# Performance work log

Hardware: AMD Instinct MI355X
Metric: run time of the kernel (lower is better)

The kernel has to match this reference:

```python
import jax, jax.numpy as jnp
import numpy as np
from jax import lax

S, U, T, F = 64, 10, 160, 80       # speakers, utterances, frames, mel features
H, P, E, L = 768, 256, 256, 3      # hidden, proj, embedding, layers


def setup_inputs() -> dict:
    key = jax.random.key(0)
    ks = iter(jax.random.split(key, 32))
    s = 0.05
    d = {"x": jax.random.normal(next(ks), (S, U, T, F), jnp.float32)}
    for l in range(L):
        fin = F if l == 0 else P
        d[f"W_ih{l}"] = jax.random.normal(next(ks), (4 * H, fin), jnp.float32) * s
        d[f"W_hh{l}"] = jax.random.normal(next(ks), (4 * H, P), jnp.float32) * s
        d[f"b_ih{l}"] = jax.random.normal(next(ks), (4 * H,), jnp.float32) * s
        d[f"b_hh{l}"] = jax.random.normal(next(ks), (4 * H,), jnp.float32) * s
        d[f"W_hr{l}"] = jax.random.normal(next(ks), (P, H), jnp.float32) * s
    d["W_lin"] = jax.random.normal(next(ks), (E, P), jnp.float32) * s
    d["b_lin"] = jax.random.normal(next(ks), (E,), jnp.float32) * s
    return d


def _lstm_layer(x, Wih, Whh, bih, bhh, Whr):
    """Projected LSTM layer (PyTorch proj_size semantics, gate order i,f,g,o).
    x: [B, T, Fin] -> (outputs [B, T, P], final h [B, P])."""
    B = x.shape[0]
    # precompute input contribution for all timesteps: [T, B, 4H]
    pre = jnp.einsum('btf,gf->tbg', x, Wih) + bih + bhh

    def step(carry, pre_t):
        h, c = carry
        g = pre_t + h @ Whh.T                     # [B, 4H]
        i, f, gg, o = jnp.split(g, 4, axis=-1)
        c = jax.nn.sigmoid(f) * c + jax.nn.sigmoid(i) * jnp.tanh(gg)
        h = (jax.nn.sigmoid(o) * jnp.tanh(c)) @ Whr.T  # project H -> P
        return (h, c), h

    init = (jnp.zeros((B, P), x.dtype), jnp.zeros((B, H), x.dtype))
    (h_last, _), hs = lax.scan(step, init, pre)
    return jnp.transpose(hs, (1, 0, 2)), h_last


def reference(x, W_ih0, W_hh0, b_ih0, b_hh0, W_hr0,
              W_ih1, W_hh1, b_ih1, b_hh1, W_hr1,
              W_ih2, W_hh2, b_ih2, b_hh2, W_hr2,
              W_lin, b_lin):
    layers = [(W_ih0, W_hh0, b_ih0, b_hh0, W_hr0),
              (W_ih1, W_hh1, b_ih1, b_hh1, W_hr1),
              (W_ih2, W_hh2, b_ih2, b_hh2, W_hr2)]
    seq = x.reshape(-1, x.shape[2], x.shape[3])  # [S*U, T, F]
    h_last = None
    for (Wih, Whh, bih, bhh, Whr) in layers:
        seq, h_last = _lstm_layer(seq, Wih, Whh, bih, bhh, Whr)
    out = jax.nn.relu(h_last @ W_lin.T + b_lin)  # [S*U, E]
    norm = jnp.linalg.norm(out, axis=1, keepdims=True)
    out = out / jnp.maximum(norm, 1e-12)         # F.normalize(p=2, dim=1)
    return out.reshape(x.shape[0], x.shape[1], -1)  # [S, U, E]
```

## Files before the change

kernel.cpp:

```cpp
#include <hip/hip_runtime.h>
#include <stdint.h>

#define Sn 64
#define Un 10
#define Tn 160
#define Fn 80
#define Bn 640
#define Hn 768
#define Pn 256
#define En 256
#define G4H 3072
#define NBLK 480

using short8  = __attribute__((ext_vector_type(8))) short;
using short4v = __attribute__((ext_vector_type(4))) short;
using floatx4 = __attribute__((ext_vector_type(4))) float;

__device__ __forceinline__ short f2bf(float f){
    unsigned u = __builtin_bit_cast(unsigned, f);
    u += 0x7fffu + ((u >> 16) & 1u);
    return (short)(u >> 16);
}
__device__ __forceinline__ float bf2f(short s){
    return __builtin_bit_cast(float, ((unsigned)(unsigned short)s) << 16);
}
__device__ __forceinline__ float sigm(float x){ return 1.f / (1.f + __expf(-x)); }
__device__ __forceinline__ float tanh_(float x){
    float e = __expf(-2.f * fmaxf(x, -40.f));
    return (1.f - e) / (1.f + e);
}

__device__ __forceinline__ void gll(const short* g, short* l){
    __builtin_amdgcn_global_load_lds(
        (const __attribute__((address_space(1))) unsigned int*)(const void*)g,
        (__attribute__((address_space(3))) unsigned int*)(void*)l, 16, 0, 0);
}
#define VMW(N) asm volatile("s_waitcnt vmcnt(" #N ")" ::: "memory")
#define LGKM0  asm volatile("s_waitcnt lgkmcnt(0)" ::: "memory")


__global__ void k_prep(const float* __restrict__ Wih0,
                       const float* bi0, const float* bh0,
                       const float* bi1, const float* bh1,
                       const float* bi2, const float* bh2,
                       short* __restrict__ B0, float* __restrict__ bias){
    int i = blockIdx.x * 256 + threadIdx.x;
    const int W0 = G4H * 96;
    if (i < W0){
        int g = i / 96, c = i % 96;
        int gg = g / 768, jj = g % 768;
        int ct = jj / 48, r = jj % 48, ntB = r / 16, lnB = r % 16;
        int k = 768 + c, s = k >> 5, lq = (k >> 3) & 3, e = k & 7;
        size_t off = ((((size_t)(ct * 27 + s)) * 4 + gg) * 3 + ntB) * 512
                   + (size_t)(lq * 16 + lnB) * 8 + e;
        B0[off] = (c < Fn) ? f2bf(Wih0[(size_t)g * Fn + c]) : (short)0;
    } else if (i < W0 + 3 * G4H){
        int j = i - W0; int l = j / G4H, g = j % G4H;
        const float* a = (l == 0) ? bi0 : (l == 1) ? bi1 : bi2;
        const float* b = (l == 0) ? bh0 : (l == 1) ? bh1 : bh2;
        bias[j] = a[g] + b[g];
    }
}

__global__ void k_init(short* __restrict__ hidden, float* __restrict__ c){
    int i = blockIdx.x * 256 + threadIdx.x;
    int stride = gridDim.x * 256;
    const int NH = 3 * 2 * Bn * Hn;
    const int NC = 3 * Bn * Hn;
    for (int j = i; j < NH; j += stride) hidden[j] = 0;
    for (int j = i; j < NC; j += stride) c[j] = 0.f;
}

__global__ void k_fold(const float* __restrict__ A, const float* __restrict__ Whr,
                       short* __restrict__ out, int ldout, int coloff, int Mtiles,
                       int nstg){
    int mt = blockIdx.x % Mtiles, nt = blockIdx.x / Mtiles;
    int lane = threadIdx.x & 63;
    int ln = lane & 15, lq = lane >> 4;
    floatx4 acc = {0.f, 0.f, 0.f, 0.f};
    const float* ap = A + (size_t)(mt * 16 + ln) * 256 + lq * 8;
    const float* bp = Whr + (size_t)(lq * 8) * 768 + nt * 16 + ln;
    for (int p0 = 0; p0 < 256; p0 += 32){
        short8 af, bf;
        #pragma unroll
        for (int j = 0; j < 8; ++j) af[j] = f2bf(ap[p0 + j]);
        #pragma unroll
        for (int j = 0; j < 8; ++j) bf[j] = f2bf(bp[(size_t)(p0 + j) * 768]);
        acc = __builtin_amdgcn_mfma_f32_16x16x32_bf16(af, bf, acc, 0, 0, 0);
    }
    #pragma unroll
    for (int r = 0; r < 4; ++r){
        int row = mt * 16 + lq * 4 + r, col = nt * 16 + ln;
        int k = coloff + col;
        if (nstg){
            int gg = row / 768, jj = row % 768;
            int ct = jj / 48, rr = jj % 48, ntB = rr / 16, lnB = rr % 16;
            int s = k >> 5, lqk = (k >> 3) & 3, e = k & 7;
            size_t off = ((((size_t)ct * nstg + s) * 4 + gg) * 3 + ntB) * 512
                       + (size_t)(lqk * 16 + lnB) * 8 + e;
            out[off] = f2bf(acc[r]);
        } else {
            out[(size_t)row * ldout + k] = f2bf(acc[r]);
        }
    }
}

__global__ __launch_bounds__(256, 2) void k_step(const float* __restrict__ x,
        const short* __restrict__ B0, const short* __restrict__ B1,
        const short* __restrict__ B2, const float* __restrict__ bias,
        short* __restrict__ hidden, float* __restrict__ c, int w){
    __shared__ __align__(16) char smem[25088];
    short* sAr = (short*)smem;
    float* sEx = (float*)smem;

    const int tid = threadIdx.x, lane = tid & 63, wg = tid >> 6;
    const int bid = blockIdx.x;
    const int layer = bid % 3;
    const int t = w - layer;
    if (t < 0 || t >= Tn) return;
    const int r2 = bid / 3;
    const int mt = r2 >> 4, ct = r2 & 15;
    const int m0 = mt * 64, j0 = ct * 48;
    const short* Bl = (layer == 0) ? B0 : (layer == 1) ? B1 : B2;
    const int NSTG = (layer == 0) ? 27 : 48;
    const int ln = lane & 15, lq = lane >> 4;
    const int rr = tid >> 2;
    const int pp = (w + 1) & 1;

    const short* bglane = Bl + (size_t)lane * 8;
    const int ctb = ct * NSTG;

    int aoffA[3];
    #pragma unroll
    for (int j = 0; j < 3; ++j){
        int u = (wg * 3 + j) * 64 + lane;
        int row = u / 12, kcp = u % 12;
        int kcg = kcp - (row % 12); if (kcg < 0) kcg += 12;
        aoffA[j] = row * 96 + kcg * 8;
    }
    int prem[4];
    #pragma unroll
    for (int m4 = 0; m4 < 4; ++m4) prem[m4] = (m4 * 16 + ln) % 12;

    const short* srcA = (layer == 0) ? hidden + (size_t)pp * Bn * Hn
                       : hidden + (size_t)((layer - 1) * 2 + pp) * Bn * Hn;
    const short* srcH = hidden + (size_t)(layer * 2 + pp) * Bn * Hn;

    short8 bfr[3][3];

#define LOADB(s_, slot_)                                                        \
    {                                                                           \
        const short* p_ = bglane + (size_t)(((ctb) + (s_)) * 12 + wg * 3) * 512;\
        asm volatile("global_load_dwordx4 %0, %1, off"                          \
                     : "=v"(bfr[slot_][0]) : "v"(p_) : "memory");               \
        asm volatile("global_load_dwordx4 %0, %1, off offset:1024"              \
                     : "=v"(bfr[slot_][1]) : "v"(p_) : "memory");               \
        asm volatile("global_load_dwordx4 %0, %1, off offset:2048"              \
                     : "=v"(bfr[slot_][2]) : "v"(p_) : "memory");               \
    }

    auto issueA = [&](int chn){
        const short* src; int chg;
        if (layer == 0 || chn < 8){ src = srcA; chg = chn; }
        else { src = srcH; chg = chn - 8; }
        const short* gb = src + (size_t)(mt * 8 + chg) * 6144;
        #pragma unroll
        for (int j = 0; j < 3; ++j)
            gll(gb + aoffA[j], &sAr[(chn & 1) * 6144 + (wg * 3 + j) * 512]);
    };

    floatx4 acc[4][3];
    #pragma unroll
    for (int nt = 0; nt < 3; ++nt){
        float bv = bias[layer * G4H + wg * Hn + j0 + nt * 16 + ln];
        #pragma unroll
        for (int m4 = 0; m4 < 4; ++m4){
            acc[m4][nt][0] = bv; acc[m4][nt][1] = bv;
            acc[m4][nt][2] = bv; acc[m4][nt][3] = bv;
        }
    }

#define PH(k_, WAITN, ISSUE)                                                    \
    {                                                                           \
        VMW(WAITN);                                                             \
        __builtin_amdgcn_sched_barrier(0);                                      \
        short8 afr[4];                                                          \
        const int ksl_ = (k_) * 4 + lq;                                         \
        _Pragma("unroll")                                                       \
        for (int m4 = 0; m4 < 4; ++m4){                                         \
            int idx = prem[m4] + ksl_; if (idx >= 12) idx -= 12;                \
            afr[m4] = *(const short8*)&sAr[abuf * 6144 + ((m4 * 16 + ln) * 12 + idx) * 8]; \
        }                                                                       \
        _Pragma("unroll")                                                       \
        for (int m4 = 0; m4 < 4; ++m4)                                          \
            _Pragma("unroll")                                                   \
            for (int nt = 0; nt < 3; ++nt)                                      \
                acc[m4][nt] = __builtin_amdgcn_mfma_f32_16x16x32_bf16(afr[m4], bfr[k_][nt], acc[m4][nt], 0, 0, 0); \
        ISSUE;                                                                  \
    }

    issueA(0);
    LOADB(0, 0); LOADB(1, 1); LOADB(2, 2);
    VMW(9);
    __builtin_amdgcn_s_barrier();

    const int NST = (layer == 0) ? 7 : 15;
    for (int ch = 0; ch < NST; ++ch){
        const int s0 = 3 * ch;
        const int abuf = ch & 1;
        issueA(ch + 1);
        PH(0, 9, LOADB(s0 + 3, 0));
        PH(1, 9, LOADB(s0 + 4, 1));
        PH(2, 9, LOADB(s0 + 5, 2));
        VMW(6);
        __builtin_amdgcn_s_barrier();
    }
    if (layer == 0){
        {
            const int abuf = 1;
            PH(0, 6, LOADB(24, 0));
            PH(1, 6, LOADB(25, 1));
            PH(2, 6, LOADB(26, 2));
            __builtin_amdgcn_s_barrier();
        }
        {
            const float* xr = x + ((size_t)(m0 + rr) * Tn + t) * Fn;
            int q3 = (tid & 3) * 3;
            #pragma unroll
            for (int ii = 0; ii < 3; ++ii){
                int kcg = q3 + ii;
                int f = kcg * 8;
                short8 v = {0,0,0,0,0,0,0,0};
                if (f < Fn){
                    float4 a = *(const float4*)(xr + f);
                    float4 b = *(const float4*)(xr + f + 4);
                    v[0]=f2bf(a.x); v[1]=f2bf(a.y); v[2]=f2bf(a.z); v[3]=f2bf(a.w);
                    v[4]=f2bf(b.x); v[5]=f2bf(b.y); v[6]=f2bf(b.z); v[7]=f2bf(b.w);
                }
                int kcp = kcg + (rr % 12); if (kcp >= 12) kcp -= 12;
                *(short8*)&sAr[(rr * 12 + kcp) * 8] = v;
            }
            LGKM0;
            __builtin_amdgcn_s_barrier();
        }
        {
            const int abuf = 0;
            PH(0, 6, (void)0);
            PH(1, 3, (void)0);
            PH(2, 0, (void)0);
            __builtin_amdgcn_s_barrier();
        }
    } else {
        {
            const int abuf = 1;
            PH(0, 6, (void)0);
            PH(1, 3, (void)0);
            PH(2, 0, (void)0);
            __builtin_amdgcn_s_barrier();
        }
    }
#undef PH
#undef LOADB

    #pragma unroll
    for (int p = 0; p < 2; ++p){
        if (p) __syncthreads();
        #pragma unroll
        for (int mm = 0; mm < 2; ++mm){
            int m4 = p * 2 + mm;
            #pragma unroll
            for (int nt = 0; nt < 3; ++nt)
                #pragma unroll
                for (int r = 0; r < 4; ++r)
                    sEx[(wg * 32 + mm * 16 + lq * 4 + r) * 49 + nt * 16 + ln] = acc[m4][nt][r];
        }
        __syncthreads();
        {
            int r32 = tid >> 3, cbp = (tid & 7) * 6;
            int row = p * 32 + r32;
            float* cp = c + ((size_t)layer * Bn + (m0 + row)) * Hn + j0 + cbp;
            short hb[6];
            #pragma unroll
            for (int ii = 0; ii < 6; ++ii){
                int cc_ = cbp + ii;
                float gi = sEx[(0 * 32 + r32) * 49 + cc_];
                float gf = sEx[(1 * 32 + r32) * 49 + cc_];
                float gg = sEx[(2 * 32 + r32) * 49 + cc_];
                float go = sEx[(3 * 32 + r32) * 49 + cc_];
                float cv = sigm(gf) * cp[ii] + sigm(gi) * tanh_(gg);
                cp[ii] = cv;
                hb[ii] = f2bf(sigm(go) * tanh_(cv));
            }
            short* hbase = hidden + (size_t)(layer * 2 + (w & 1)) * Bn * Hn;
            short* hp = hbase + ((size_t)((mt * 8 + (ct >> 1)) * 64 + row) * 96
                                 + (ct & 1) * 48 + cbp);
            #pragma unroll
            for (int q = 0; q < 3; ++q){
                unsigned v = (unsigned)(unsigned short)hb[q * 2] |
                             ((unsigned)(unsigned short)hb[q * 2 + 1] << 16);
                *(unsigned*)&hp[q * 2] = v;
            }
        }
    }
}

__global__ void k_final(const short* __restrict__ h2, const short* __restrict__ Wf,
                        const float* __restrict__ blin, float* __restrict__ out){
    __shared__ __align__(16) short sH[768];
    __shared__ float sW[4];
    int b = blockIdx.x, e = threadIdx.x;
    if (e < 96){
        int mtb = b >> 6, rowb = b & 63;
        *(short8*)&sH[e * 8] = *(const short8*)
            &h2[((size_t)(mtb * 8 + e / 12) * 64 + rowb) * 96 + (e % 12) * 8];
    }
    __syncthreads();
    float acc = blin[e];
    const short* wr = Wf + (size_t)e * 768;
    for (int j = 0; j < 768; j += 8){
        short8 hv = *(const short8*)&sH[j];
        short8 wv = *(const short8*)&wr[j];
        #pragma unroll
        for (int k = 0; k < 8; ++k) acc += bf2f(hv[k]) * bf2f(wv[k]);
    }
    float v = fmaxf(acc, 0.f);
    float s = v * v;
    #pragma unroll
    for (int off = 32; off >= 1; off >>= 1) s += __shfl_down(s, off);
    if ((e & 63) == 0) sW[e >> 6] = s;
    __syncthreads();
    float tot = sW[0] + sW[1] + sW[2] + sW[3];
    float scale = 1.f / fmaxf(sqrtf(tot), 1e-12f);
    out[(size_t)b * 256 + e] = v * scale;
}

extern "C" void kernel_launch(void* const* d_in, const int* in_sizes, int n_in,
                              void* d_out, int out_size, void* d_ws, size_t ws_size,
                              hipStream_t stream){
    const float* x    = (const float*)d_in[0];
    const float* Wih0 = (const float*)d_in[1];
    const float* Whh0 = (const float*)d_in[2];
    const float* bi0  = (const float*)d_in[3];
    const float* bh0  = (const float*)d_in[4];
    const float* Whr0 = (const float*)d_in[5];
    const float* Wih1 = (const float*)d_in[6];
    const float* Whh1 = (const float*)d_in[7];
    const float* bi1  = (const float*)d_in[8];
    const float* bh1  = (const float*)d_in[9];
    const float* Whr1 = (const float*)d_in[10];
    const float* Wih2 = (const float*)d_in[11];
    const float* Whh2 = (const float*)d_in[12];
    const float* bi2  = (const float*)d_in[13];
    const float* bh2  = (const float*)d_in[14];
    const float* Whr2 = (const float*)d_in[15];
    const float* Wlin = (const float*)d_in[16];
    const float* blin = (const float*)d_in[17];

    char* wp = (char*)d_ws;
    size_t off = 0;
    auto alloc = [&](size_t bytes) -> char* {
        char* p = wp + off; off += (bytes + 255) & ~(size_t)255; return p;
    };
    short* B0   = (short*)alloc((size_t)G4H * 864 * 2);
    short* B1   = (short*)alloc((size_t)G4H * 1536 * 2);
    short* B2   = (short*)alloc((size_t)G4H * 1536 * 2);
    short* Wf   = (short*)alloc((size_t)256 * 768 * 2);
    float* bias = (float*)alloc((size_t)3 * G4H * 4);
    short* hid  = (short*)alloc((size_t)3 * 2 * Bn * Hn * 2);
    float* cst  = (float*)alloc((size_t)3 * Bn * Hn * 4);

    hipLaunchKernelGGL(k_prep, dim3(1188), dim3(256), 0, stream,
                       Wih0, bi0, bh0, bi1, bh1, bi2, bh2, B0, bias);
    hipLaunchKernelGGL(k_init, dim3(1024), dim3(256), 0, stream, hid, cst);
    hipLaunchKernelGGL(k_fold, dim3(192 * 48), dim3(64), 0, stream, Whh0, Whr0, B0, 0, 0,   192, 27);
    hipLaunchKernelGGL(k_fold, dim3(192 * 48), dim3(64), 0, stream, Wih1, Whr0, B1, 0, 0,   192, 48);
    hipLaunchKernelGGL(k_fold, dim3(192 * 48), dim3(64), 0, stream, Whh1, Whr1, B1, 0, 768, 192, 48);
    hipLaunchKernelGGL(k_fold, dim3(192 * 48), dim3(64), 0, stream, Wih2, Whr1, B2, 0, 0,   192, 48);
    hipLaunchKernelGGL(k_fold, dim3(192 * 48), dim3(64), 0, stream, Whh2, Whr2, B2, 0, 768, 192, 48);
    hipLaunchKernelGGL(k_fold, dim3(16 * 48), dim3(64), 0, stream, Wlin, Whr2, Wf, 768, 0, 16, 0);

    for (int w = 0; w < 162; ++w)
        hipLaunchKernelGGL(k_step, dim3(NBLK), dim3(256), 0, stream,
                           x, B0, B1, B2, bias, hid, cst, w);

    const short* h2 = hid + (size_t)5 * Bn * Hn;
    hipLaunchKernelGGL(k_final, dim3(Bn), dim3(256), 0, stream, h2, Wf, blin, (float*)d_out);
}
```

Before: 4.066 ms.

## Double row tile to 128 and split K across two 256-thread halves

Each k_step block now covers 128 batch rows instead of 64 and runs 512 threads. The two groups of four waves each take half of the K chunks (split-K) and combine their partial gate sums in LDS before the LSTM cell update. This halves the block count to 240, so each fetched weight tile is reused across twice as many rows and B-matrix global traffic drops. In exchange each block uses 96KB of LDS and more accumulator registers, which lowers occupancy, and layer 0 splits its K range unevenly between the two halves.

```diff
diff --git a/kernel.cpp b/kernel.cpp
--- a/kernel.cpp
+++ b/kernel.cpp
@@ -10,10 +10,9 @@
 #define Pn 256
 #define En 256
 #define G4H 3072
-#define NBLK 480
+#define NBLK 240
 
 using short8  = __attribute__((ext_vector_type(8))) short;
-using short4v = __attribute__((ext_vector_type(4))) short;
 using floatx4 = __attribute__((ext_vector_type(4))) float;
 
 __device__ __forceinline__ short f2bf(float f){
@@ -105,42 +104,42 @@
     }
 }
 
-__global__ __launch_bounds__(256, 2) void k_step(const float* __restrict__ x,
+__global__ __launch_bounds__(512, 2) void k_step(const float* __restrict__ x,
         const short* __restrict__ B0, const short* __restrict__ B1,
         const short* __restrict__ B2, const float* __restrict__ bias,
         short* __restrict__ hidden, float* __restrict__ c, int w){
-    __shared__ __align__(16) char smem[25088];
+    __shared__ __align__(16) char smem[98304];
     short* sAr = (short*)smem;
     float* sEx = (float*)smem;
 
-    const int tid = threadIdx.x, lane = tid & 63, wg = tid >> 6;
+    const int tid = threadIdx.x, lane = tid & 63;
+    const int wg = (tid >> 6) & 3, kh = tid >> 8;
     const int bid = blockIdx.x;
     const int layer = bid % 3;
     const int t = w - layer;
     if (t < 0 || t >= Tn) return;
     const int r2 = bid / 3;
     const int mt = r2 >> 4, ct = r2 & 15;
-    const int m0 = mt * 64, j0 = ct * 48;
+    const int m0 = mt * 128, j0 = ct * 48;
     const short* Bl = (layer == 0) ? B0 : (layer == 1) ? B1 : B2;
     const int NSTG = (layer == 0) ? 27 : 48;
     const int ln = lane & 15, lq = lane >> 4;
-    const int rr = tid >> 2;
     const int pp = (w + 1) & 1;
 
     const short* bglane = Bl + (size_t)lane * 8;
     const int ctb = ct * NSTG;
 
-    int aoffA[3];
-    #pragma unroll
-    for (int j = 0; j < 3; ++j){
-        int u = (wg * 3 + j) * 64 + lane;
+    int aoffA[6];
+    #pragma unroll
+    for (int j = 0; j < 6; ++j){
+        int u = (wg * 6 + j) * 64 + lane;
         int row = u / 12, kcp = u % 12;
         int kcg = kcp - (row % 12); if (kcg < 0) kcg += 12;
         aoffA[j] = row * 96 + kcg * 8;
     }
-    int prem[4];
-    #pragma unroll
-    for (int m4 = 0; m4 < 4; ++m4) prem[m4] = (m4 * 16 + ln) % 12;
+    int prem[8];
+    #pragma unroll
+    for (int m8 = 0; m8 < 8; ++m8) prem[m8] = (m8 * 16 + ln) % 12;
 
     const short* srcA = (layer == 0) ? hidden + (size_t)pp * Bn * Hn
                        : hidden + (size_t)((layer - 1) * 2 + pp) * Bn * Hn;
@@ -163,73 +162,72 @@
         const short* src; int chg;
         if (layer == 0 || chn < 8){ src = srcA; chg = chn; }
         else { src = srcH; chg = chn - 8; }
-        const short* gb = src + (size_t)(mt * 8 + chg) * 6144;
-        #pragma unroll
-        for (int j = 0; j < 3; ++j)
-            gll(gb + aoffA[j], &sAr[(chn & 1) * 6144 + (wg * 3 + j) * 512]);
+        const short* gb = src + (size_t)(mt * 8 + chg) * 12288;
+        short* db = &sAr[(size_t)(2 * kh + (chn & 1)) * 12288];
+        #pragma unroll
+        for (int j = 0; j < 6; ++j)
+            gll(gb + aoffA[j], db + (wg * 6 + j) * 512);
     };
 
-    floatx4 acc[4][3];
+    floatx4 acc[8][3];
     #pragma unroll
     for (int nt = 0; nt < 3; ++nt){
-        float bv = bias[layer * G4H + wg * Hn + j0 + nt * 16 + ln];
-        #pragma unroll
-        for (int m4 = 0; m4 < 4; ++m4){
-            acc[m4][nt][0] = bv; acc[m4][nt][1] = bv;
-            acc[m4][nt][2] = bv; acc[m4][nt][3] = bv;
-        }
-    }
-
-#define PH(k_, WAITN, ISSUE)                                                    \
+        float bv = (kh == 0) ? bias[layer * G4H + wg * Hn + j0 + nt * 16 + ln] : 0.f;
+        #pragma unroll
+        for (int m8 = 0; m8 < 8; ++m8){
+            acc[m8][nt][0] = bv; acc[m8][nt][1] = bv;
+            acc[m8][nt][2] = bv; acc[m8][nt][3] = bv;
+        }
+    }
+
+#define PH(k_, AB_, WAITN, ISSUE)                                               \
     {                                                                           \
         VMW(WAITN);                                                             \
         __builtin_amdgcn_sched_barrier(0);                                      \
-        short8 afr[4];                                                          \
+        short8 afr[8];                                                          \
         const int ksl_ = (k_) * 4 + lq;                                         \
         _Pragma("unroll")                                                       \
-        for (int m4 = 0; m4 < 4; ++m4){                                         \
-            int idx = prem[m4] + ksl_; if (idx >= 12) idx -= 12;                \
-            afr[m4] = *(const short8*)&sAr[abuf * 6144 + ((m4 * 16 + ln) * 12 + idx) * 8]; \
+        for (int m8 = 0; m8 < 8; ++m8){                                         \
+            int idx = prem[m8] + ksl_; if (idx >= 12) idx -= 12;                \
+            afr[m8] = *(const short8*)&sAr[(size_t)(AB_) * 12288 + ((m8 * 16 + ln) * 12 + idx) * 8]; \
         }                                                                       \
         _Pragma("unroll")                                                       \
-        for (int m4 = 0; m4 < 4; ++m4)                                          \
+        for (int m8 = 0; m8 < 8; ++m8)                                          \
             _Pragma("unroll")                                                   \
             for (int nt = 0; nt < 3; ++nt)                                      \
-                acc[m4][nt] = __builtin_amdgcn_mfma_f32_16x16x32_bf16(afr[m4], bfr[k_][nt], acc[m4][nt], 0, 0, 0); \
+                acc[m8][nt] = __builtin_amdgcn_mfma_f32_16x16x32_bf16(afr[m8], bfr[k_][nt], acc[m8][nt], 0, 0, 0); \
         ISSUE;                                                                  \
     }
 
-    issueA(0);
-    LOADB(0, 0); LOADB(1, 1); LOADB(2, 2);
+    const int c0 = (kh == 0) ? 0 : ((layer == 0) ? 5 : 8);
+    issueA(c0);
+    LOADB(3 * c0 + 0, 0); LOADB(3 * c0 + 1, 1); LOADB(3 * c0 + 2, 2);
     VMW(9);
     __builtin_amdgcn_s_barrier();
 
-    const int NST = (layer == 0) ? 7 : 15;
-    for (int ch = 0; ch < NST; ++ch){
-        const int s0 = 3 * ch;
-        const int abuf = ch & 1;
+    const int NSTD = (kh == 0) ? ((layer == 0) ? 4 : 7)
+                               : ((layer == 0) ? 2 : 7);
+    for (int i = 0; i < NSTD; ++i){
+        const int ch = c0 + i, s0 = 3 * ch;
+        const int ab = 2 * kh + (ch & 1);
         issueA(ch + 1);
-        PH(0, 9, LOADB(s0 + 3, 0));
-        PH(1, 9, LOADB(s0 + 4, 1));
-        PH(2, 9, LOADB(s0 + 5, 2));
-        VMW(6);
-        __builtin_amdgcn_s_barrier();
-    }
-    if (layer == 0){
+        PH(0, ab, 12, LOADB(s0 + 3, 0));
+        PH(1, ab, 12, LOADB(s0 + 4, 1));
+        PH(2, ab, 12, LOADB(s0 + 5, 2));
+        VMW(9);
+        __builtin_amdgcn_s_barrier();
+    }
+    if (layer == 0 && kh == 1){
+        PH(0, 3, 6, LOADB(24, 0));
+        PH(1, 3, 6, LOADB(25, 1));
+        PH(2, 3, 6, LOADB(26, 2));
+        __builtin_amdgcn_s_barrier();
         {
-            const int abuf = 1;
-            PH(0, 6, LOADB(24, 0));
-            PH(1, 6, LOADB(25, 1));
-            PH(2, 6, LOADB(26, 2));
-            __builtin_amdgcn_s_barrier();
-        }
-        {
-            const float* xr = x + ((size_t)(m0 + rr) * Tn + t) * Fn;
-            int q3 = (tid & 3) * 3;
+            int l = tid & 255, rrx = l >> 1, q6 = (l & 1) * 6;
+            const float* xr = x + ((size_t)(m0 + rrx) * Tn + t) * Fn;
             #pragma unroll
-            for (int ii = 0; ii < 3; ++ii){
-                int kcg = q3 + ii;
-                int f = kcg * 8;
+            for (int ii = 0; ii < 6; ++ii){
+                int kcg = q6 + ii, f = kcg * 8;
                 short8 v = {0,0,0,0,0,0,0,0};
                 if (f < Fn){
                     float4 a = *(const float4*)(xr + f);
@@ -237,68 +235,61 @@
                     v[0]=f2bf(a.x); v[1]=f2bf(a.y); v[2]=f2bf(a.z); v[3]=f2bf(a.w);
                     v[4]=f2bf(b.x); v[5]=f2bf(b.y); v[6]=f2bf(b.z); v[7]=f2bf(b.w);
                 }
-                int kcp = kcg + (rr % 12); if (kcp >= 12) kcp -= 12;
-                *(short8*)&sAr[(rr * 12 + kcp) * 8] = v;
+                int kcp = kcg + (rrx % 12); if (kcp >= 12) kcp -= 12;
+                *(short8*)&sAr[2 * 12288 + (rrx * 12 + kcp) * 8] = v;
             }
             LGKM0;
             __builtin_amdgcn_s_barrier();
         }
-        {
-            const int abuf = 0;
-            PH(0, 6, (void)0);
-            PH(1, 3, (void)0);
-            PH(2, 0, (void)0);
-            __builtin_amdgcn_s_barrier();
-        }
+        PH(0, 2, 6, (void)0);
+        PH(1, 2, 3, (void)0);
+        PH(2, 2, 0, (void)0);
+        __builtin_amdgcn_s_barrier();
+    } else if (layer == 0 && kh == 0){
+        PH(0, 0, 6, (void)0);
+        PH(1, 0, 3, (void)0);
+        PH(2, 0, 0, (void)0);
+        __builtin_amdgcn_s_barrier();
     } else {
-        {
-            const int abuf = 1;
-            PH(0, 6, (void)0);
-            PH(1, 3, (void)0);
-            PH(2, 0, (void)0);
-            __builtin_amdgcn_s_barrier();
-        }
+        const int ab = 2 * kh + 1;
+        PH(0, ab, 6, (void)0);
+        PH(1, ab, 3, (void)0);
+        PH(2, ab, 0, (void)0);
+        __builtin_amdgcn_s_barrier();
     }
 #undef PH
 #undef LOADB
 
     #pragma unroll
-    for (int p = 0; p < 2; ++p){
+    for (int p = 0; p < 4; ++p){
         if (p) __syncthreads();
         #pragma unroll
         for (int mm = 0; mm < 2; ++mm){
-            int m4 = p * 2 + mm;
             #pragma unroll
             for (int nt = 0; nt < 3; ++nt)
                 #pragma unroll
                 for (int r = 0; r < 4; ++r)
-                    sEx[(wg * 32 + mm * 16 + lq * 4 + r) * 49 + nt * 16 + ln] = acc[m4][nt][r];
+                    sEx[((size_t)(kh * 4 + wg) * 32 + mm * 16 + lq * 4 + r) * 49
+                        + nt * 16 + ln] = acc[2 * p + mm][nt][r];
         }
         __syncthreads();
         {
-            int r32 = tid >> 3, cbp = (tid & 7) * 6;
+            int r32 = tid >> 4, cb3 = (tid & 15) * 3;
             int row = p * 32 + r32;
-            float* cp = c + ((size_t)layer * Bn + (m0 + row)) * Hn + j0 + cbp;
-            short hb[6];
+            float* cp = c + ((size_t)layer * Bn + (m0 + row)) * Hn + j0 + cb3;
+            short* hbase = hidden + (size_t)(layer * 2 + (w & 1)) * Bn * Hn;
+            short* hp = hbase + ((size_t)(mt * 8 + (ct >> 1)) * 128 + row) * 96
+                      + (ct & 1) * 48 + cb3;
             #pragma unroll
-            for (int ii = 0; ii < 6; ++ii){
-                int cc_ = cbp + ii;
-                float gi = sEx[(0 * 32 + r32) * 49 + cc_];
-                float gf = sEx[(1 * 32 + r32) * 49 + cc_];
-                float gg = sEx[(2 * 32 + r32) * 49 + cc_];
-                float go = sEx[(3 * 32 + r32) * 49 + cc_];
+            for (int ii = 0; ii < 3; ++ii){
+                int cc_ = cb3 + ii;
+                float gi = sEx[(0 * 32 + r32) * 49 + cc_] + sEx[(4 * 32 + r32) * 49 + cc_];
+                float gf = sEx[(1 * 32 + r32) * 49 + cc_] + sEx[(5 * 32 + r32) * 49 + cc_];
+                float gg = sEx[(2 * 32 + r32) * 49 + cc_] + sEx[(6 * 32 + r32) * 49 + cc_];
+                float go = sEx[(3 * 32 + r32) * 49 + cc_] + sEx[(7 * 32 + r32) * 49 + cc_];
                 float cv = sigm(gf) * cp[ii] + sigm(gi) * tanh_(gg);
                 cp[ii] = cv;
-                hb[ii] = f2bf(sigm(go) * tanh_(cv));
-            }
-            short* hbase = hidden + (size_t)(layer * 2 + (w & 1)) * Bn * Hn;
-            short* hp = hbase + ((size_t)((mt * 8 + (ct >> 1)) * 64 + row) * 96
-                                 + (ct & 1) * 48 + cbp);
-            #pragma unroll
-            for (int q = 0; q < 3; ++q){
-                unsigned v = (unsigned)(unsigned short)hb[q * 2] |
-                             ((unsigned)(unsigned short)hb[q * 2 + 1] << 16);
-                *(unsigned*)&hp[q * 2] = v;
+                hp[ii] = f2bf(sigm(go) * tanh_(cv));
             }
         }
     }
@@ -310,9 +301,9 @@
     __shared__ float sW[4];
     int b = blockIdx.x, e = threadIdx.x;
     if (e < 96){
-        int mtb = b >> 6, rowb = b & 63;
+        int mtb = b >> 7, rowb = b & 127;
         *(short8*)&sH[e * 8] = *(const short8*)
-            &h2[((size_t)(mtb * 8 + e / 12) * 64 + rowb) * 96 + (e % 12) * 8];
+            &h2[((size_t)(mtb * 8 + e / 12) * 128 + rowb) * 96 + (e % 12) * 8];
     }
     __syncthreads();
     float acc = blin[e];
@@ -380,7 +371,7 @@
     hipLaunchKernelGGL(k_fold, dim3(16 * 48), dim3(64), 0, stream, Wlin, Whr2, Wf, 768, 0, 16, 0);
 
     for (int w = 0; w < 162; ++w)
-        hipLaunchKernelGGL(k_step, dim3(NBLK), dim3(256), 0, stream,
+        hipLaunchKernelGGL(k_step, dim3(NBLK), dim3(512), 0, stream,
                            x, B0, B1, B2, bias, hid, cst, w);
 
     const short* h2 = hid + (size_t)5 * Bn * Hn;
```

New measurement: 4.988 ms. +22.7%, slower.
